# Kernel tuning notes

Measured on AMD Instinct MI355X. Metric: run time of the kernel, lower is better.

The kernel has to match this reference:

```python
import jax, jax.numpy as jnp
import numpy as np

T, H, I, E, TOP_K = 4096, 2048, 768, 16, 2


def _pack_i2s(tern):
    # tern: int8 in {-1,0,1}, shape [..., K] with K % 4 == 0
    m = (tern + 1).astype(jnp.uint8)  # map to {0,1,2}
    m = m.reshape(*tern.shape[:-1], -1, 4)
    return (m[..., 0] | (m[..., 1] << 2) | (m[..., 2] << 4) | (m[..., 3] << 6)).astype(jnp.uint8)


def _quantize_alpha(alpha):
    # per-column alpha -> int8 with global scale (quantize_alpha_int8)
    scale = jnp.maximum(jnp.abs(alpha).max(), 1e-8) / 127.0
    q = jnp.clip(jnp.round(alpha / scale), -128, 127).astype(jnp.int8)
    return q, scale.astype(jnp.float32)


def _unpack_i2s(packed, K, alpha):
    # packed: uint8 [..., N, K//4]; alpha: [..., K] per input column
    shifts = jnp.array([0, 2, 4, 6], dtype=jnp.uint8)
    ext = (packed[..., None] >> shifts) & jnp.uint8(3)  # [..., N, K//4, 4]
    vals = ext.reshape(*packed.shape[:-1], K).astype(jnp.float32) - 1.0  # {-1,0,1}
    return vals * alpha[..., None, :]


def setup_inputs() -> dict:
    key = jax.random.key(0)
    ks = jax.random.split(key, 6)
    x = jax.random.normal(ks[0], (T, H), dtype=jnp.float32)
    router_logits = jax.random.normal(ks[1], (T, E), dtype=jnp.float32)
    tern13 = jax.random.randint(ks[2], (E, 2 * I, H), -1, 2, dtype=jnp.int8)
    tern2 = jax.random.randint(ks[3], (E, H, I), -1, 2, dtype=jnp.int8)
    a13 = jax.random.uniform(ks[4], (E, H), minval=0.01, maxval=0.05, dtype=jnp.float32)
    a2 = jax.random.uniform(ks[5], (E, I), minval=0.01, maxval=0.05, dtype=jnp.float32)
    w13_alpha_q, w13_alpha_scale = _quantize_alpha(a13)
    w2_alpha_q, w2_alpha_scale = _quantize_alpha(a2)
    return {
        "x": x,
        "router_logits": router_logits,
        "w13_packed": _pack_i2s(tern13),
        "w13_alpha_q": w13_alpha_q,
        "w13_alpha_scale": w13_alpha_scale,
        "w2_packed": _pack_i2s(tern2),
        "w2_alpha_q": w2_alpha_q,
        "w2_alpha_scale": w2_alpha_scale,
    }


def reference(x, router_logits, w13_packed, w13_alpha_q, w13_alpha_scale,
              w2_packed, w2_alpha_q, w2_alpha_scale):
    # dequant int8 alphas, then dequant 2-bit ternary weights
    a13 = w13_alpha_q.astype(jnp.float32) * w13_alpha_scale  # [E, H]
    a2 = w2_alpha_q.astype(jnp.float32) * w2_alpha_scale     # [E, I]
    w13 = _unpack_i2s(w13_packed, H, a13)  # [E, 2I, H]
    w2 = _unpack_i2s(w2_packed, I, a2)     # [E, H, I]

    # top-k routing with renormalized softmax weights
    probs = jax.nn.softmax(router_logits, axis=-1)
    topw, topi = jax.lax.top_k(probs, TOP_K)           # [T, k]
    topw = topw / topw.sum(axis=-1, keepdims=True)
    combine = jnp.sum(jax.nn.one_hot(topi, E, dtype=x.dtype) * topw[..., None], axis=1)  # [T, E]

    # grouped expert matmuls (dense dispatch over experts)
    gu = jnp.einsum('th,enh->ten', x, w13)             # [T, E, 2I]
    gate, up = jnp.split(gu, 2, axis=-1)
    act = jax.nn.silu(gate) * up                       # [T, E, I]
    down = jnp.einsum('tei,ehi->teh', act, w2)         # [T, E, H]
    return jnp.einsum('te,teh->th', combine, down)     # [T, H]
```

## Files before the change

kernel.cpp:

```cpp
#include <hip/hip_runtime.h>
#include <stdint.h>

#define T_TOK 4096
#define HDIM  2048
#define IDIM  768
#define NEXP  16
#define NPAIR (T_TOK * 2)
#define PAIR_CAP (NPAIR + 256)

typedef float f32x4 __attribute__((ext_vector_type(4)));
typedef __bf16 bf16x8 __attribute__((ext_vector_type(8)));
typedef unsigned short u16x8 __attribute__((ext_vector_type(8)));
typedef unsigned int u32;
typedef const __attribute__((address_space(1))) u32* as1_u32p;
typedef __attribute__((address_space(3))) u32* as3_u32p;

__device__ __forceinline__ unsigned short f2bf(float f) {
  u32 u = __float_as_uint(f);
  u += 0x7FFFu + ((u >> 16) & 1u);
  return (unsigned short)(u >> 16);
}

__device__ __forceinline__ f32x4 mfma16(bf16x8 a, bf16x8 b, f32x4 c) {
  return __builtin_amdgcn_mfma_f32_16x16x32_bf16(a, b, c, 0, 0, 0);
}

__device__ __forceinline__ void stage16(unsigned short* dst, u32 w) {
  u32 o[8];
#pragma unroll
  for (int i = 0; i < 4; ++i) {
    const u32 t  = (w >> (2 * i)) & 0x03030303u;
    const u32 hb = __builtin_amdgcn_perm(0u, 0x003F00BFu, t);
    const u32 lb = __builtin_amdgcn_perm(0u, 0x00800080u, t);
    o[2 * i]     = __builtin_amdgcn_perm(hb, lb, 0x05010400u);
    o[2 * i + 1] = __builtin_amdgcn_perm(hb, lb, 0x07030602u);
  }
  *(uint4*)(dst + 0) = make_uint4(o[0], o[1], o[2], o[3]);
  *(uint4*)(dst + 8) = make_uint4(o[4], o[5], o[6], o[7]);
}

__global__ __launch_bounds__(256) void route_kernel(
    const float* __restrict__ logits, int* __restrict__ counts,
    int* __restrict__ t2i, float* __restrict__ t2w) {
  const int t = blockIdx.x * 256 + threadIdx.x;
  if (t >= T_TOK) return;
  const float* l = logits + t * NEXP;
  float m0 = -1e30f, m1 = -1e30f;
  int i0 = 0, i1 = 0;
#pragma unroll
  for (int j = 0; j < NEXP; ++j) {
    const float v = l[j];
    if (v > m0) { m1 = m0; i1 = i0; m0 = v; i0 = j; }
    else if (v > m1) { m1 = v; i1 = j; }
  }
  const float w0 = 1.0f / (1.0f + expf(m1 - m0));
  t2i[t] = i0 | (i1 << 8);
  t2w[t] = w0;
  atomicAdd(&counts[i0], 1);
  atomicAdd(&counts[i1], 1);
}

__global__ void scan_kernel(const int* __restrict__ counts,
                            int* __restrict__ offs, int* __restrict__ cursor) {
  if (threadIdx.x == 0) {
    int s = 0;
    for (int e = 0; e < NEXP; ++e) { offs[e] = s; cursor[e] = s; s += counts[e]; }
    offs[NEXP] = s;
  }
}

__global__ __launch_bounds__(256) void fill_kernel(
    const int* __restrict__ t2i, const float* __restrict__ t2w,
    int* __restrict__ cursor, int* __restrict__ pair_token,
    float* __restrict__ pair_wt, int* __restrict__ pair_eid,
    int* __restrict__ t2p0, int* __restrict__ t2p1) {
  const int t = blockIdx.x * 256 + threadIdx.x;
  if (t >= T_TOK) return;
  const int ii = t2i[t];
  const float w0 = t2w[t];
  const int i0 = ii & 255, i1 = (ii >> 8) & 255;
  const int p0 = atomicAdd(&cursor[i0], 1);
  pair_token[p0] = t; pair_wt[p0] = w0; pair_eid[p0] = i0;
  const int p1 = atomicAdd(&cursor[i1], 1);
  pair_token[p1] = t; pair_wt[p1] = 1.0f - w0; pair_eid[p1] = i1;
  t2p0[t] = p0; t2p1[t] = p1;
}

__global__ __launch_bounds__(256) void repack_kernel(
    const int* __restrict__ w, u32* __restrict__ o) {
  const int j0 = (blockIdx.x * 256 + threadIdx.x) * 4;
  const int4* w4 = (const int4*)w;
  uint4 r;
#pragma unroll
  for (int k = 0; k < 4; ++k) {
    const int4 a = w4[j0 + k];
    u32 x = (u32)(a.x & 255) | ((u32)(a.y & 255) << 8) |
            ((u32)(a.z & 255) << 16) | ((u32)(a.w & 255) << 24);
    u32 t = (x ^ (x >> 12)) & 0x0000F0F0u; x ^= t ^ (t << 12);
    t = (x ^ (x >> 6)) & 0x00CC00CCu;      x ^= t ^ (t << 6);
    ((u32*)&r)[k] = x;
  }
  ((uint4*)o)[blockIdx.x * 256 + threadIdx.x] = r;
}

__global__ __launch_bounds__(256) void xg_kernel(
    const float* __restrict__ x, const int* __restrict__ a13q,
    const float* __restrict__ s13p, const int* __restrict__ pair_token,
    const int* __restrict__ pair_eid, unsigned short* __restrict__ xg) {
  const int p = blockIdx.x;
  const int t = pair_token[p];
  const int e = pair_eid[p];
  const float s13 = *s13p;
  const int h0 = threadIdx.x * 8;
  const float* xp = x + (size_t)t * HDIM + h0;
  const int* ap = a13q + (size_t)e * HDIM + h0;
  const float4 x0 = ((const float4*)xp)[0];
  const float4 x1 = ((const float4*)xp)[1];
  const int4 a0 = ((const int4*)ap)[0];
  const int4 a1 = ((const int4*)ap)[1];
  u16x8 q;
  q[0] = f2bf(x0.x * (float)a0.x * s13);
  q[1] = f2bf(x0.y * (float)a0.y * s13);
  q[2] = f2bf(x0.z * (float)a0.z * s13);
  q[3] = f2bf(x0.w * (float)a0.w * s13);
  q[4] = f2bf(x1.x * (float)a1.x * s13);
  q[5] = f2bf(x1.y * (float)a1.y * s13);
  q[6] = f2bf(x1.z * (float)a1.z * s13);
  q[7] = f2bf(x1.w * (float)a1.w * s13);
  *(u16x8*)(xg + (size_t)p * HDIM + h0) = q;
}

__global__ __launch_bounds__(256, 4) void gemm1_kernel(
    const u32* __restrict__ wq13, const int* __restrict__ a2q,
    const float* __restrict__ s2p, const int* __restrict__ counts,
    const int* __restrict__ offs, const float* __restrict__ pair_wt,
    const unsigned short* __restrict__ xg, unsigned short* __restrict__ act) {
  const int id = blockIdx.x;
  const int xcd = id & 7, sblk = id >> 3;
  const int nT = sblk % 12;
  const int gg = (sblk / 12) * 8 + xcd;
  const int e = gg & 15, mT = gg >> 4;
  const int cnt = counts[e];
  if (mT * 128 >= cnt) return;
  const int base = offs[e];
  const int tid = threadIdx.x;

  __shared__ __align__(16) unsigned short sA0[128 * 32];
  __shared__ __align__(16) unsigned short sA1[128 * 32];
  __shared__ __align__(16) unsigned short sB0[128 * 40];
  __shared__ __align__(16) unsigned short sB1[128 * 40];

  const int wave = tid >> 6, lane = tid & 63;
  const int wm = wave >> 1, wn = wave & 1;
  const int quad = lane >> 4, ln = lane & 15;

  const int bn = tid >> 1, bhalf = tid & 1;
  const int grow = (bn < 64) ? (nT * 64 + bn) : (IDIM + nT * 64 + (bn - 64));
  const u32* browp = wq13 + ((size_t)e * (2 * IDIM) + grow) * (HDIM / 16);
  const int sBoff = bn * 40 + (bhalf << 4);

  const int arow = lane >> 2;
  const int acol = (lane & 3) * 8;
  const size_t arow0 = (size_t)(base + mT * 128);

  f32x4 acc[4][4] = {};

#define G1_MFMA(sAx, sBx)                                                          \
  {                                                                                \
    bf16x8 af[4];                                                                  \
    _Pragma("unroll") for (int mi = 0; mi < 4; ++mi)                               \
        af[mi] = *(const bf16x8*)(sAx + (wm * 64 + mi * 16 + ln) * 32 + quad * 8); \
    bf16x8 b0 = *(const bf16x8*)(sBx + (wn * 32 + ln) * 40 + quad * 8);            \
    bf16x8 b1 = *(const bf16x8*)(sBx + (wn * 32 + 16 + ln) * 40 + quad * 8);       \
    bf16x8 b2 = *(const bf16x8*)(sBx + (64 + wn * 32 + ln) * 40 + quad * 8);       \
    bf16x8 b3 = *(const bf16x8*)(sBx + (64 + wn * 32 + 16 + ln) * 40 + quad * 8);  \
    _Pragma("unroll") for (int mi = 0; mi < 4; ++mi) {                             \
      acc[mi][0] = mfma16(af[mi], b0, acc[mi][0]);                                 \
      acc[mi][1] = mfma16(af[mi], b1, acc[mi][1]);                                 \
      acc[mi][2] = mfma16(af[mi], b2, acc[mi][2]);                                 \
      acc[mi][3] = mfma16(af[mi], b3, acc[mi][3]);                                 \
    }                                                                              \
  }

  uint4 W = *(const uint4*)(browp);
  for (int s = 0; s < HDIM / 64; ++s) {
#pragma unroll
    for (int c = 0; c < 2; ++c) {
      const unsigned short* gp =
          xg + (arow0 + wave * 32 + c * 16 + arow) * HDIM + s * 64 + acol;
      unsigned short* lp = sA0 + (wave * 32 + c * 16) * 32;
      __builtin_amdgcn_global_load_lds((as1_u32p)(const void*)gp, (as3_u32p)(void*)lp, 16, 0, 0);
    }
#pragma unroll
    for (int c = 0; c < 2; ++c) {
      const unsigned short* gp =
          xg + (arow0 + wave * 32 + c * 16 + arow) * HDIM + s * 64 + 32 + acol;
      unsigned short* lp = sA1 + (wave * 32 + c * 16) * 32;
      __builtin_amdgcn_global_load_lds((as1_u32p)(const void*)gp, (as3_u32p)(void*)lp, 16, 0, 0);
    }
    const int sn = (s + 1 < HDIM / 64) ? s + 1 : s;
    const uint4 Wn = *(const uint4*)(browp + 4 * sn);
    stage16(sB0 + sBoff, bhalf ? W.y : W.x);
    stage16(sB1 + sBoff, bhalf ? W.w : W.z);
    __syncthreads();
    G1_MFMA(sA0, sB0);
    G1_MFMA(sA1, sB1);
    __syncthreads();
    W = Wn;
  }

  const float s2 = *s2p;
#pragma unroll
  for (int gi = 0; gi < 2; ++gi) {
    const int i = nT * 64 + wn * 32 + gi * 16 + ln;
    const float a2v = (float)a2q[e * IDIM + i] * s2;
#pragma unroll
    for (int mi = 0; mi < 4; ++mi) {
      const f32x4 g = acc[mi][gi];
      const f32x4 u = acc[mi][gi + 2];
#pragma unroll
      for (int r = 0; r < 4; ++r) {
        const int m = mT * 128 + wm * 64 + mi * 16 + quad * 4 + r;
        if (m < cnt) {
          const float wt = pair_wt[base + m];
          const float gv = g[r];
          const float av = gv / (1.0f + __expf(-gv)) * u[r] * a2v * wt;
          act[(size_t)(base + m) * IDIM + i] = f2bf(av);
        }
      }
    }
  }
}

__global__ __launch_bounds__(256, 4) void gemm2_kernel(
    const u32* __restrict__ wq2, const int* __restrict__ counts,
    const int* __restrict__ offs, const unsigned short* __restrict__ act,
    unsigned short* __restrict__ down) {
  const int id = blockIdx.x;
  const int xcd = id & 7, sblk = id >> 3;
  const int nT = sblk & 15;
  const int gg = (sblk >> 4) * 8 + xcd;
  const int e = gg & 15, mT = gg >> 4;
  const int cnt = counts[e];
  if (mT * 128 >= cnt) return;
  const int base = offs[e];
  const int tid = threadIdx.x;

  __shared__ __align__(16) unsigned short sA0[128 * 32];
  __shared__ __align__(16) unsigned short sA1[128 * 32];
  __shared__ __align__(16) unsigned short sB0[128 * 40];
  __shared__ __align__(16) unsigned short sB1[128 * 40];

  const int wave = tid >> 6, lane = tid & 63;
  const int wm = wave >> 1, wn = wave & 1;
  const int quad = lane >> 4, ln = lane & 15;

  const int bn = tid >> 1, bhalf = tid & 1;
  const u32* browp = wq2 + ((size_t)e * HDIM + nT * 128 + bn) * (IDIM / 16);
  const int sBoff = bn * 40 + (bhalf << 4);

  const int arow = lane >> 2;
  const int acol = (lane & 3) * 8;
  const size_t arow0 = (size_t)(base + mT * 128);

  f32x4 acc[4][4] = {};

#define G2_MFMA(sAx, sBx)                                                          \
  {                                                                                \
    bf16x8 af[4];                                                                  \
    _Pragma("unroll") for (int mi = 0; mi < 4; ++mi)                               \
        af[mi] = *(const bf16x8*)(sAx + (wm * 64 + mi * 16 + ln) * 32 + quad * 8); \
    bf16x8 b0 = *(const bf16x8*)(sBx + (wn * 64 + ln) * 40 + quad * 8);            \
    bf16x8 b1 = *(const bf16x8*)(sBx + (wn * 64 + 16 + ln) * 40 + quad * 8);       \
    bf16x8 b2 = *(const bf16x8*)(sBx + (wn * 64 + 32 + ln) * 40 + quad * 8);       \
    bf16x8 b3 = *(const bf16x8*)(sBx + (wn * 64 + 48 + ln) * 40 + quad * 8);       \
    _Pragma("unroll") for (int mi = 0; mi < 4; ++mi) {                             \
      acc[mi][0] = mfma16(af[mi], b0, acc[mi][0]);                                 \
      acc[mi][1] = mfma16(af[mi], b1, acc[mi][1]);                                 \
      acc[mi][2] = mfma16(af[mi], b2, acc[mi][2]);                                 \
      acc[mi][3] = mfma16(af[mi], b3, acc[mi][3]);                                 \
    }                                                                              \
  }

  uint4 W = *(const uint4*)(browp);
  for (int s = 0; s < IDIM / 64; ++s) {
#pragma unroll
    for (int c = 0; c < 2; ++c) {
      const unsigned short* gp =
          act + (arow0 + wave * 32 + c * 16 + arow) * IDIM + s * 64 + acol;
      unsigned short* lp = sA0 + (wave * 32 + c * 16) * 32;
      __builtin_amdgcn_global_load_lds((as1_u32p)(const void*)gp, (as3_u32p)(void*)lp, 16, 0, 0);
    }
#pragma unroll
    for (int c = 0; c < 2; ++c) {
      const unsigned short* gp =
          act + (arow0 + wave * 32 + c * 16 + arow) * IDIM + s * 64 + 32 + acol;
      unsigned short* lp = sA1 + (wave * 32 + c * 16) * 32;
      __builtin_amdgcn_global_load_lds((as1_u32p)(const void*)gp, (as3_u32p)(void*)lp, 16, 0, 0);
    }
    const int sn = (s + 1 < IDIM / 64) ? s + 1 : s;
    const uint4 Wn = *(const uint4*)(browp + 4 * sn);
    stage16(sB0 + sBoff, bhalf ? W.y : W.x);
    stage16(sB1 + sBoff, bhalf ? W.w : W.z);
    __syncthreads();
    G2_MFMA(sA0, sB0);
    G2_MFMA(sA1, sB1);
    __syncthreads();
    W = Wn;
  }

#pragma unroll
  for (int mi = 0; mi < 4; ++mi) {
#pragma unroll
    for (int r = 0; r < 4; ++r) {
      const int ml = wm * 64 + mi * 16 + quad * 4 + r;
      const int m = mT * 128 + ml;
      if (m < cnt) {
        unsigned short* drow = down + (size_t)(base + m) * HDIM + nT * 128 + wn * 64;
#pragma unroll
        for (int ni = 0; ni < 4; ++ni)
          drow[ni * 16 + ln] = f2bf(acc[mi][ni][r]);
      }
    }
  }
}

__global__ __launch_bounds__(256) void combine_kernel(
    const int* __restrict__ t2p0, const int* __restrict__ t2p1,
    const unsigned short* __restrict__ down, float* __restrict__ out) {
  const int t = blockIdx.x;
  const int h = threadIdx.x * 8;
  const u16x8 a = *(const u16x8*)(down + (size_t)t2p0[t] * HDIM + h);
  const u16x8 b = *(const u16x8*)(down + (size_t)t2p1[t] * HDIM + h);
  f32x4 o0, o1;
#pragma unroll
  for (int j = 0; j < 4; ++j) {
    o0[j] = __uint_as_float((u32)a[j] << 16) + __uint_as_float((u32)b[j] << 16);
    o1[j] = __uint_as_float((u32)a[j + 4] << 16) + __uint_as_float((u32)b[j + 4] << 16);
  }
  float* o = out + (size_t)t * HDIM + h;
  *(f32x4*)(o) = o0;
  *(f32x4*)(o + 4) = o1;
}

extern "C" void kernel_launch(void* const* d_in, const int* in_sizes, int n_in,
                              void* d_out, int out_size, void* d_ws, size_t ws_size,
                              hipStream_t stream) {
  const float* x      = (const float*)d_in[0];
  const float* logits = (const float*)d_in[1];
  const int*   w13p   = (const int*)d_in[2];
  const int*   a13q   = (const int*)d_in[3];
  const float* s13    = (const float*)d_in[4];
  const int*   w2p    = (const int*)d_in[5];
  const int*   a2q    = (const int*)d_in[6];
  const float* s2     = (const float*)d_in[7];
  float* out = (float*)d_out;

  char* ws = (char*)d_ws;
  int*   counts     = (int*)(ws + 0);
  int*   cursor     = (int*)(ws + 64);
  int*   offs       = (int*)(ws + 128);
  int*   t2i        = (int*)(ws + 256);
  float* t2w        = (float*)(ws + 256 + 4 * T_TOK);
  int*   t2p0       = (int*)(ws + 256 + 8 * T_TOK);
  int*   t2p1       = (int*)(ws + 256 + 12 * T_TOK);
  int*   pair_token = (int*)(ws + 256 + 16 * T_TOK);
  float* pair_wt    = (float*)(ws + 256 + 16 * T_TOK + 4 * PAIR_CAP);
  int*   pair_eid   = (int*)(ws + 256 + 16 * T_TOK + 8 * PAIR_CAP);
  const size_t hdr_end = ((size_t)(256 + 16 * T_TOK + 12 * PAIR_CAP) + 255) & ~(size_t)255;

  const size_t n32_13 = (size_t)NEXP * 2 * IDIM * (HDIM / 16);
  const size_t n32_2  = (size_t)NEXP * HDIM * (IDIM / 16);
  const size_t rp13_b = n32_13 * 4, rp2_b = n32_2 * 4;
  const size_t xg_b   = (size_t)PAIR_CAP * HDIM * 2;

  u32* rp13 = (u32*)(ws + hdr_end);
  u32* rp2  = (u32*)(ws + hdr_end + rp13_b);
  unsigned short* xg  = (unsigned short*)(ws + hdr_end + rp13_b + rp2_b);
  unsigned short* act = (unsigned short*)(ws + hdr_end + rp13_b + rp2_b + xg_b);
  unsigned short* down = xg;

  hipMemsetAsync(counts, 0, 256, stream);
  route_kernel<<<T_TOK / 256, 256, 0, stream>>>(logits, counts, t2i, t2w);
  scan_kernel<<<1, 64, 0, stream>>>(counts, offs, cursor);
  fill_kernel<<<T_TOK / 256, 256, 0, stream>>>(t2i, t2w, cursor, pair_token, pair_wt,
                                               pair_eid, t2p0, t2p1);
  repack_kernel<<<(int)(n32_13 / 1024), 256, 0, stream>>>(w13p, rp13);
  repack_kernel<<<(int)(n32_2 / 1024), 256, 0, stream>>>(w2p, rp2);
  xg_kernel<<<NPAIR, 256, 0, stream>>>(x, a13q, s13, pair_token, pair_eid, xg);

  gemm1_kernel<<<6144, 256, 0, stream>>>(rp13, a2q, s2, counts, offs, pair_wt, xg, act);
  gemm2_kernel<<<8192, 256, 0, stream>>>(rp2, counts, offs, act, down);
  combine_kernel<<<T_TOK, 256, 0, stream>>>(t2p0, t2p1, down, out);
}
```

Baseline: 335.6 us.

## Expand ternary B fragments in registers and double-buffer A tiles in LDS

Both expert GEMM kernels stop staging decoded ternary weights through shared memory. Each lane now loads the packed words it needs and expands them straight into MFMA B fragments, which removes the LDS write/read round trip for B and one barrier per step. The LDS saved is spent on double-buffering the activation tiles: the async global-to-LDS copy for the next K step is issued before the current step's MFMAs, and s_setprio raises the priority of the MFMA block. In exchange, each wave reloads and re-expands weight rows that other waves also use, and register pressure rises, so the launch bound drops from 4 to 3 blocks per CU.

```diff
diff --git a/kernel.cpp b/kernel.cpp
--- a/kernel.cpp
+++ b/kernel.cpp
@@ -12,6 +12,7 @@
 typedef __bf16 bf16x8 __attribute__((ext_vector_type(8)));
 typedef unsigned short u16x8 __attribute__((ext_vector_type(8)));
 typedef unsigned int u32;
+typedef u32 u32x4 __attribute__((ext_vector_type(4)));
 typedef const __attribute__((address_space(1))) u32* as1_u32p;
 typedef __attribute__((address_space(3))) u32* as3_u32p;
 
@@ -25,18 +26,20 @@
   return __builtin_amdgcn_mfma_f32_16x16x32_bf16(a, b, c, 0, 0, 0);
 }
 
-__device__ __forceinline__ void stage16(unsigned short* dst, u32 w) {
-  u32 o[8];
-#pragma unroll
-  for (int i = 0; i < 4; ++i) {
-    const u32 t  = (w >> (2 * i)) & 0x03030303u;
-    const u32 hb = __builtin_amdgcn_perm(0u, 0x003F00BFu, t);
-    const u32 lb = __builtin_amdgcn_perm(0u, 0x00800080u, t);
-    o[2 * i]     = __builtin_amdgcn_perm(hb, lb, 0x05010400u);
-    o[2 * i + 1] = __builtin_amdgcn_perm(hb, lb, 0x07030602u);
-  }
-  *(uint4*)(dst + 0) = make_uint4(o[0], o[1], o[2], o[3]);
-  *(uint4*)(dst + 8) = make_uint4(o[4], o[5], o[6], o[7]);
+__device__ __forceinline__ bf16x8 expand8(u32 w, int qshift) {
+  w >>= qshift;
+  const u32 t0 = w & 0x03030303u;
+  const u32 h0 = __builtin_amdgcn_perm(0u, 0x003F00BFu, t0);
+  const u32 l0 = __builtin_amdgcn_perm(0u, 0x00800080u, t0);
+  const u32 t1 = (w >> 2) & 0x03030303u;
+  const u32 h1 = __builtin_amdgcn_perm(0u, 0x003F00BFu, t1);
+  const u32 l1 = __builtin_amdgcn_perm(0u, 0x00800080u, t1);
+  u32x4 o;
+  o[0] = __builtin_amdgcn_perm(h0, l0, 0x05010400u);
+  o[1] = __builtin_amdgcn_perm(h0, l0, 0x07030602u);
+  o[2] = __builtin_amdgcn_perm(h1, l1, 0x05010400u);
+  o[3] = __builtin_amdgcn_perm(h1, l1, 0x07030602u);
+  return __builtin_bit_cast(bf16x8, o);
 }
 
 __global__ __launch_bounds__(256) void route_kernel(
@@ -130,7 +133,59 @@
   *(u16x8*)(xg + (size_t)p * HDIM + h0) = q;
 }
 
-__global__ __launch_bounds__(256, 4) void gemm1_kernel(
+#define DMA_A(src, pitch, dst0, dst1, sidx)                                          \
+  {                                                                                  \
+    _Pragma("unroll") for (int c = 0; c < 2; ++c) {                                  \
+      const unsigned short* gp =                                                     \
+          src + (arow0 + wave * 32 + c * 16 + arow) * (pitch) + (sidx) * 64 + acol;  \
+      unsigned short* lp = dst0 + (wave * 32 + c * 16) * 32;                         \
+      __builtin_amdgcn_global_load_lds((as1_u32p)(const void*)gp,                    \
+                                       (as3_u32p)(void*)lp, 16, 0, 0);               \
+    }                                                                                \
+    _Pragma("unroll") for (int c = 0; c < 2; ++c) {                                  \
+      const unsigned short* gp =                                                     \
+          src + (arow0 + wave * 32 + c * 16 + arow) * (pitch) + (sidx) * 64 + 32 +   \
+          acol;                                                                      \
+      unsigned short* lp = dst1 + (wave * 32 + c * 16) * 32;                         \
+      __builtin_amdgcn_global_load_lds((as1_u32p)(const void*)gp,                    \
+                                       (as3_u32p)(void*)lp, 16, 0, 0);               \
+    }                                                                                \
+  }
+
+#define LOADW(W0, W1, W2, W3, sidx)            \
+  {                                            \
+    W0 = *(const uint4*)(rp0 + (sidx) * 4);    \
+    W1 = *(const uint4*)(rp1 + (sidx) * 4);    \
+    W2 = *(const uint4*)(rp2 + (sidx) * 4);    \
+    W3 = *(const uint4*)(rp3 + (sidx) * 4);    \
+  }
+
+#define MKFRAGS(fr, W0, W1, W2, W3)                       \
+  {                                                       \
+    fr[0] = expand8(qsel ? W0.y : W0.x, qshift);          \
+    fr[1] = expand8(qsel ? W1.y : W1.x, qshift);          \
+    fr[2] = expand8(qsel ? W2.y : W2.x, qshift);          \
+    fr[3] = expand8(qsel ? W3.y : W3.x, qshift);          \
+    fr[4] = expand8(qsel ? W0.w : W0.z, qshift);          \
+    fr[5] = expand8(qsel ? W1.w : W1.z, qshift);          \
+    fr[6] = expand8(qsel ? W2.w : W2.z, qshift);          \
+    fr[7] = expand8(qsel ? W3.w : W3.z, qshift);          \
+  }
+
+#define MFMA4(sAx, b0, b1, b2, b3)                                                  \
+  {                                                                                 \
+    bf16x8 af[4];                                                                   \
+    _Pragma("unroll") for (int mi = 0; mi < 4; ++mi)                                \
+        af[mi] = *(const bf16x8*)(sAx + (wm * 64 + mi * 16 + ln) * 32 + quad * 8);  \
+    _Pragma("unroll") for (int mi = 0; mi < 4; ++mi) {                              \
+      acc[mi][0] = mfma16(af[mi], b0, acc[mi][0]);                                  \
+      acc[mi][1] = mfma16(af[mi], b1, acc[mi][1]);                                  \
+      acc[mi][2] = mfma16(af[mi], b2, acc[mi][2]);                                  \
+      acc[mi][3] = mfma16(af[mi], b3, acc[mi][3]);                                  \
+    }                                                                               \
+  }
+
+__global__ __launch_bounds__(256, 3) void gemm1_kernel(
     const u32* __restrict__ wq13, const int* __restrict__ a2q,
     const float* __restrict__ s2p, const int* __restrict__ counts,
     const int* __restrict__ offs, const float* __restrict__ pair_wt,
@@ -145,19 +200,19 @@
   const int base = offs[e];
   const int tid = threadIdx.x;
 
-  __shared__ __align__(16) unsigned short sA0[128 * 32];
-  __shared__ __align__(16) unsigned short sA1[128 * 32];
-  __shared__ __align__(16) unsigned short sB0[128 * 40];
-  __shared__ __align__(16) unsigned short sB1[128 * 40];
+  __shared__ __align__(16) unsigned short sA[2][2][128 * 32];
 
   const int wave = tid >> 6, lane = tid & 63;
   const int wm = wave >> 1, wn = wave & 1;
   const int quad = lane >> 4, ln = lane & 15;
-
-  const int bn = tid >> 1, bhalf = tid & 1;
-  const int grow = (bn < 64) ? (nT * 64 + bn) : (IDIM + nT * 64 + (bn - 64));
-  const u32* browp = wq13 + ((size_t)e * (2 * IDIM) + grow) * (HDIM / 16);
-  const int sBoff = bn * 40 + (bhalf << 4);
+  const int qsel = quad >> 1;
+  const int qshift = (quad & 1) * 4;
+
+  const size_t rstride = HDIM / 16;
+  const u32* rp0 = wq13 + ((size_t)e * (2 * IDIM) + nT * 64 + wn * 32 + ln) * rstride;
+  const u32* rp1 = rp0 + 16 * rstride;
+  const u32* rp2 = rp0 + (size_t)IDIM * rstride;
+  const u32* rp3 = rp2 + 16 * rstride;
 
   const int arow = lane >> 2;
   const int acol = (lane & 3) * 8;
@@ -165,55 +220,45 @@
 
   f32x4 acc[4][4] = {};
 
-#define G1_MFMA(sAx, sBx)                                                          \
-  {                                                                                \
-    bf16x8 af[4];                                                                  \
-    _Pragma("unroll") for (int mi = 0; mi < 4; ++mi)                               \
-        af[mi] = *(const bf16x8*)(sAx + (wm * 64 + mi * 16 + ln) * 32 + quad * 8); \
-    bf16x8 b0 = *(const bf16x8*)(sBx + (wn * 32 + ln) * 40 + quad * 8);            \
-    bf16x8 b1 = *(const bf16x8*)(sBx + (wn * 32 + 16 + ln) * 40 + quad * 8);       \
-    bf16x8 b2 = *(const bf16x8*)(sBx + (64 + wn * 32 + ln) * 40 + quad * 8);       \
-    bf16x8 b3 = *(const bf16x8*)(sBx + (64 + wn * 32 + 16 + ln) * 40 + quad * 8);  \
-    _Pragma("unroll") for (int mi = 0; mi < 4; ++mi) {                             \
-      acc[mi][0] = mfma16(af[mi], b0, acc[mi][0]);                                 \
-      acc[mi][1] = mfma16(af[mi], b1, acc[mi][1]);                                 \
-      acc[mi][2] = mfma16(af[mi], b2, acc[mi][2]);                                 \
-      acc[mi][3] = mfma16(af[mi], b3, acc[mi][3]);                                 \
-    }                                                                              \
-  }
-
-  uint4 W = *(const uint4*)(browp);
-  for (int s = 0; s < HDIM / 64; ++s) {
-#pragma unroll
-    for (int c = 0; c < 2; ++c) {
-      const unsigned short* gp =
-          xg + (arow0 + wave * 32 + c * 16 + arow) * HDIM + s * 64 + acol;
-      unsigned short* lp = sA0 + (wave * 32 + c * 16) * 32;
-      __builtin_amdgcn_global_load_lds((as1_u32p)(const void*)gp, (as3_u32p)(void*)lp, 16, 0, 0);
-    }
-#pragma unroll
-    for (int c = 0; c < 2; ++c) {
-      const unsigned short* gp =
-          xg + (arow0 + wave * 32 + c * 16 + arow) * HDIM + s * 64 + 32 + acol;
-      unsigned short* lp = sA1 + (wave * 32 + c * 16) * 32;
-      __builtin_amdgcn_global_load_lds((as1_u32p)(const void*)gp, (as3_u32p)(void*)lp, 16, 0, 0);
-    }
-    const int sn = (s + 1 < HDIM / 64) ? s + 1 : s;
-    const uint4 Wn = *(const uint4*)(browp + 4 * sn);
-    stage16(sB0 + sBoff, bhalf ? W.y : W.x);
-    stage16(sB1 + sBoff, bhalf ? W.w : W.z);
-    __syncthreads();
-    G1_MFMA(sA0, sB0);
-    G1_MFMA(sA1, sB1);
-    __syncthreads();
-    W = Wn;
-  }
-
-  const float s2 = *s2p;
+  DMA_A(xg, HDIM, sA[0][0], sA[0][1], 0);
+  uint4 WA0, WA1, WA2, WA3, WB0, WB1, WB2, WB3;
+  LOADW(WA0, WA1, WA2, WA3, 0);
+  LOADW(WB0, WB1, WB2, WB3, 1);
+
+  const int S2 = (HDIM / 64) / 2;
+  for (int s2 = 0; s2 < S2; ++s2) {
+    const int s = 2 * s2;
+    {
+      bf16x8 fr[8];
+      MKFRAGS(fr, WA0, WA1, WA2, WA3);
+      __syncthreads();
+      DMA_A(xg, HDIM, sA[1][0], sA[1][1], s + 1);
+      if (s2 + 1 < S2) LOADW(WA0, WA1, WA2, WA3, s + 2);
+      __builtin_amdgcn_s_setprio(1);
+      MFMA4(sA[0][0], fr[0], fr[1], fr[2], fr[3]);
+      MFMA4(sA[0][1], fr[4], fr[5], fr[6], fr[7]);
+      __builtin_amdgcn_s_setprio(0);
+    }
+    {
+      bf16x8 fr[8];
+      MKFRAGS(fr, WB0, WB1, WB2, WB3);
+      __syncthreads();
+      if (s2 + 1 < S2) {
+        DMA_A(xg, HDIM, sA[0][0], sA[0][1], s + 2);
+        LOADW(WB0, WB1, WB2, WB3, s + 3);
+      }
+      __builtin_amdgcn_s_setprio(1);
+      MFMA4(sA[1][0], fr[0], fr[1], fr[2], fr[3]);
+      MFMA4(sA[1][1], fr[4], fr[5], fr[6], fr[7]);
+      __builtin_amdgcn_s_setprio(0);
+    }
+  }
+
+  const float s2v = *s2p;
 #pragma unroll
   for (int gi = 0; gi < 2; ++gi) {
     const int i = nT * 64 + wn * 32 + gi * 16 + ln;
-    const float a2v = (float)a2q[e * IDIM + i] * s2;
+    const float a2v = (float)a2q[e * IDIM + i] * s2v;
 #pragma unroll
     for (int mi = 0; mi < 4; ++mi) {
       const f32x4 g = acc[mi][gi];
@@ -232,7 +277,7 @@
   }
 }
 
-__global__ __launch_bounds__(256, 4) void gemm2_kernel(
+__global__ __launch_bounds__(256, 3) void gemm2_kernel(
     const u32* __restrict__ wq2, const int* __restrict__ counts,
     const int* __restrict__ offs, const unsigned short* __restrict__ act,
     unsigned short* __restrict__ down) {
@@ -246,18 +291,19 @@
   const int base = offs[e];
   const int tid = threadIdx.x;
 
-  __shared__ __align__(16) unsigned short sA0[128 * 32];
-  __shared__ __align__(16) unsigned short sA1[128 * 32];
-  __shared__ __align__(16) unsigned short sB0[128 * 40];
-  __shared__ __align__(16) unsigned short sB1[128 * 40];
+  __shared__ __align__(16) unsigned short sA[2][2][128 * 32];
 
   const int wave = tid >> 6, lane = tid & 63;
   const int wm = wave >> 1, wn = wave & 1;
   const int quad = lane >> 4, ln = lane & 15;
-
-  const int bn = tid >> 1, bhalf = tid & 1;
-  const u32* browp = wq2 + ((size_t)e * HDIM + nT * 128 + bn) * (IDIM / 16);
-  const int sBoff = bn * 40 + (bhalf << 4);
+  const int qsel = quad >> 1;
+  const int qshift = (quad & 1) * 4;
+
+  const size_t rstride = IDIM / 16;
+  const u32* rp0 = wq2 + ((size_t)e * HDIM + nT * 128 + wn * 64 + ln) * rstride;
+  const u32* rp1 = rp0 + 16 * rstride;
+  const u32* rp2 = rp0 + 32 * rstride;
+  const u32* rp3 = rp0 + 48 * rstride;
 
   const int arow = lane >> 2;
   const int acol = (lane & 3) * 8;
@@ -265,48 +311,38 @@
 
   f32x4 acc[4][4] = {};
 
-#define G2_MFMA(sAx, sBx)                                                          \
-  {                                                                                \
-    bf16x8 af[4];                                                                  \
-    _Pragma("unroll") for (int mi = 0; mi < 4; ++mi)                               \
-        af[mi] = *(const bf16x8*)(sAx + (wm * 64 + mi * 16 + ln) * 32 + quad * 8); \
-    bf16x8 b0 = *(const bf16x8*)(sBx + (wn * 64 + ln) * 40 + quad * 8);            \
-    bf16x8 b1 = *(const bf16x8*)(sBx + (wn * 64 + 16 + ln) * 40 + quad * 8);       \
-    bf16x8 b2 = *(const bf16x8*)(sBx + (wn * 64 + 32 + ln) * 40 + quad * 8);       \
-    bf16x8 b3 = *(const bf16x8*)(sBx + (wn * 64 + 48 + ln) * 40 + quad * 8);       \
-    _Pragma("unroll") for (int mi = 0; mi < 4; ++mi) {                             \
-      acc[mi][0] = mfma16(af[mi], b0, acc[mi][0]);                                 \
-      acc[mi][1] = mfma16(af[mi], b1, acc[mi][1]);                                 \
-      acc[mi][2] = mfma16(af[mi], b2, acc[mi][2]);                                 \
-      acc[mi][3] = mfma16(af[mi], b3, acc[mi][3]);                                 \
-    }                                                                              \
-  }
-
-  uint4 W = *(const uint4*)(browp);
-  for (int s = 0; s < IDIM / 64; ++s) {
-#pragma unroll
-    for (int c = 0; c < 2; ++c) {
-      const unsigned short* gp =
-          act + (arow0 + wave * 32 + c * 16 + arow) * IDIM + s * 64 + acol;
-      unsigned short* lp = sA0 + (wave * 32 + c * 16) * 32;
-      __builtin_amdgcn_global_load_lds((as1_u32p)(const void*)gp, (as3_u32p)(void*)lp, 16, 0, 0);
-    }
-#pragma unroll
-    for (int c = 0; c < 2; ++c) {
-      const unsigned short* gp =
-          act + (arow0 + wave * 32 + c * 16 + arow) * IDIM + s * 64 + 32 + acol;
-      unsigned short* lp = sA1 + (wave * 32 + c * 16) * 32;
-      __builtin_amdgcn_global_load_lds((as1_u32p)(const void*)gp, (as3_u32p)(void*)lp, 16, 0, 0);
-    }
-    const int sn = (s + 1 < IDIM / 64) ? s + 1 : s;
-    const uint4 Wn = *(const uint4*)(browp + 4 * sn);
-    stage16(sB0 + sBoff, bhalf ? W.y : W.x);
-    stage16(sB1 + sBoff, bhalf ? W.w : W.z);
-    __syncthreads();
-    G2_MFMA(sA0, sB0);
-    G2_MFMA(sA1, sB1);
-    __syncthreads();
-    W = Wn;
+  DMA_A(act, IDIM, sA[0][0], sA[0][1], 0);
+  uint4 WA0, WA1, WA2, WA3, WB0, WB1, WB2, WB3;
+  LOADW(WA0, WA1, WA2, WA3, 0);
+  LOADW(WB0, WB1, WB2, WB3, 1);
+
+  const int S2 = (IDIM / 64) / 2;
+  for (int s2 = 0; s2 < S2; ++s2) {
+    const int s = 2 * s2;
+    {
+      bf16x8 fr[8];
+      MKFRAGS(fr, WA0, WA1, WA2, WA3);
+      __syncthreads();
+      DMA_A(act, IDIM, sA[1][0], sA[1][1], s + 1);
+      if (s2 + 1 < S2) LOADW(WA0, WA1, WA2, WA3, s + 2);
+      __builtin_amdgcn_s_setprio(1);
+      MFMA4(sA[0][0], fr[0], fr[1], fr[2], fr[3]);
+      MFMA4(sA[0][1], fr[4], fr[5], fr[6], fr[7]);
+      __builtin_amdgcn_s_setprio(0);
+    }
+    {
+      bf16x8 fr[8];
+      MKFRAGS(fr, WB0, WB1, WB2, WB3);
+      __syncthreads();
+      if (s2 + 1 < S2) {
+        DMA_A(act, IDIM, sA[0][0], sA[0][1], s + 2);
+        LOADW(WB0, WB1, WB2, WB3, s + 3);
+      }
+      __builtin_amdgcn_s_setprio(1);
+      MFMA4(sA[1][0], fr[0], fr[1], fr[2], fr[3]);
+      MFMA4(sA[1][1], fr[4], fr[5], fr[6], fr[7]);
+      __builtin_amdgcn_s_setprio(0);
+    }
   }
 
 #pragma unroll
```

Measured after the change: 386.7 us. +15.2%, slower.

## Double-buffer A tiles with async LDS DMA and raise MFMA priority in both GEMMs

Applied to the files above, without the earlier changes.

Both expert GEMM kernels now double-buffer the activation A tiles in LDS. The next k-step's global_load_lds DMA is issued right after the barrier, so it overlaps with the current step's MFMAs instead of being waited on in the same iteration. The MFMA sections are wrapped in s_setprio to favour the matrix work, and occupancy hints change from launch_bounds(256,4) to waves_per_eu(3,3). The extra A buffer adds 16KB of LDS per block, which may reduce resident blocks per CU.

```diff
diff --git a/kernel.cpp b/kernel.cpp
--- a/kernel.cpp
+++ b/kernel.cpp
@@ -12,6 +12,7 @@
 typedef __bf16 bf16x8 __attribute__((ext_vector_type(8)));
 typedef unsigned short u16x8 __attribute__((ext_vector_type(8)));
 typedef unsigned int u32;
+typedef u32 u32x4 __attribute__((ext_vector_type(4)));
 typedef const __attribute__((address_space(1))) u32* as1_u32p;
 typedef __attribute__((address_space(3))) u32* as3_u32p;
 
@@ -130,40 +131,28 @@
   *(u16x8*)(xg + (size_t)p * HDIM + h0) = q;
 }
 
-__global__ __launch_bounds__(256, 4) void gemm1_kernel(
-    const u32* __restrict__ wq13, const int* __restrict__ a2q,
-    const float* __restrict__ s2p, const int* __restrict__ counts,
-    const int* __restrict__ offs, const float* __restrict__ pair_wt,
-    const unsigned short* __restrict__ xg, unsigned short* __restrict__ act) {
-  const int id = blockIdx.x;
-  const int xcd = id & 7, sblk = id >> 3;
-  const int nT = sblk % 12;
-  const int gg = (sblk / 12) * 8 + xcd;
-  const int e = gg & 15, mT = gg >> 4;
-  const int cnt = counts[e];
-  if (mT * 128 >= cnt) return;
-  const int base = offs[e];
-  const int tid = threadIdx.x;
-
-  __shared__ __align__(16) unsigned short sA0[128 * 32];
-  __shared__ __align__(16) unsigned short sA1[128 * 32];
-  __shared__ __align__(16) unsigned short sB0[128 * 40];
-  __shared__ __align__(16) unsigned short sB1[128 * 40];
-
-  const int wave = tid >> 6, lane = tid & 63;
-  const int wm = wave >> 1, wn = wave & 1;
-  const int quad = lane >> 4, ln = lane & 15;
-
-  const int bn = tid >> 1, bhalf = tid & 1;
-  const int grow = (bn < 64) ? (nT * 64 + bn) : (IDIM + nT * 64 + (bn - 64));
-  const u32* browp = wq13 + ((size_t)e * (2 * IDIM) + grow) * (HDIM / 16);
-  const int sBoff = bn * 40 + (bhalf << 4);
-
-  const int arow = lane >> 2;
-  const int acol = (lane & 3) * 8;
-  const size_t arow0 = (size_t)(base + mT * 128);
-
-  f32x4 acc[4][4] = {};
+#define DMA_A(src, pitch, dst0, dst1, sidx)                                          \
+  {                                                                                  \
+    _Pragma("unroll") for (int c = 0; c < 2; ++c) {                                  \
+      const unsigned short* gp =                                                     \
+          src + (arow0 + wave * 32 + c * 16 + arow) * (pitch) + (sidx) * 64 + acol;  \
+      unsigned short* lp = dst0 + (wave * 32 + c * 16) * 32;                         \
+      __builtin_amdgcn_global_load_lds((as1_u32p)(const void*)gp,                    \
+                                       (as3_u32p)(void*)lp, 16, 0, 0);               \
+    }                                                                                \
+    _Pragma("unroll") for (int c = 0; c < 2; ++c) {                                  \
+      const unsigned short* gp =                                                     \
+          src + (arow0 + wave * 32 + c * 16 + arow) * (pitch) + (sidx) * 64 + 32 +   \
+          acol;                                                                      \
+      unsigned short* lp = dst1 + (wave * 32 + c * 16) * 32;                         \
+      __builtin_amdgcn_global_load_lds((as1_u32p)(const void*)gp,                    \
+                                       (as3_u32p)(void*)lp, 16, 0, 0);               \
+    }                                                                                \
+  }
+
+#define STAGE(W)                                   \
+  stage16(sB0 + sBoff, bhalf ? (W).y : (W).x);     \
+  stage16(sB1 + sBoff, bhalf ? (W).w : (W).z);
 
 #define G1_MFMA(sAx, sBx)                                                          \
   {                                                                                \
@@ -182,38 +171,79 @@
     }                                                                              \
   }
 
-  uint4 W = *(const uint4*)(browp);
-  for (int s = 0; s < HDIM / 64; ++s) {
-#pragma unroll
-    for (int c = 0; c < 2; ++c) {
-      const unsigned short* gp =
-          xg + (arow0 + wave * 32 + c * 16 + arow) * HDIM + s * 64 + acol;
-      unsigned short* lp = sA0 + (wave * 32 + c * 16) * 32;
-      __builtin_amdgcn_global_load_lds((as1_u32p)(const void*)gp, (as3_u32p)(void*)lp, 16, 0, 0);
-    }
-#pragma unroll
-    for (int c = 0; c < 2; ++c) {
-      const unsigned short* gp =
-          xg + (arow0 + wave * 32 + c * 16 + arow) * HDIM + s * 64 + 32 + acol;
-      unsigned short* lp = sA1 + (wave * 32 + c * 16) * 32;
-      __builtin_amdgcn_global_load_lds((as1_u32p)(const void*)gp, (as3_u32p)(void*)lp, 16, 0, 0);
-    }
-    const int sn = (s + 1 < HDIM / 64) ? s + 1 : s;
-    const uint4 Wn = *(const uint4*)(browp + 4 * sn);
-    stage16(sB0 + sBoff, bhalf ? W.y : W.x);
-    stage16(sB1 + sBoff, bhalf ? W.w : W.z);
-    __syncthreads();
-    G1_MFMA(sA0, sB0);
-    G1_MFMA(sA1, sB1);
-    __syncthreads();
-    W = Wn;
-  }
-
-  const float s2 = *s2p;
+__attribute__((amdgpu_waves_per_eu(3, 3))) __global__ __launch_bounds__(256)
+void gemm1_kernel(
+    const u32* __restrict__ wq13, const int* __restrict__ a2q,
+    const float* __restrict__ s2p, const int* __restrict__ counts,
+    const int* __restrict__ offs, const float* __restrict__ pair_wt,
+    const unsigned short* __restrict__ xg, unsigned short* __restrict__ act) {
+  const int id = blockIdx.x;
+  const int xcd = id & 7, sblk = id >> 3;
+  const int nT = sblk % 12;
+  const int gg = (sblk / 12) * 8 + xcd;
+  const int e = gg & 15, mT = gg >> 4;
+  const int cnt = counts[e];
+  if (mT * 128 >= cnt) return;
+  const int base = offs[e];
+  const int tid = threadIdx.x;
+
+  __shared__ __align__(16) unsigned short sA[2][2][128 * 32];
+  __shared__ __align__(16) unsigned short sB0[128 * 40 + 8];
+  __shared__ __align__(16) unsigned short sB1[128 * 40 + 8];
+
+  const int wave = tid >> 6, lane = tid & 63;
+  const int wm = wave >> 1, wn = wave & 1;
+  const int quad = lane >> 4, ln = lane & 15;
+
+  const int bn = tid >> 1, bhalf = tid & 1;
+  const int grow = (bn < 64) ? (nT * 64 + bn) : (IDIM + nT * 64 + (bn - 64));
+  const u32* browp = wq13 + ((size_t)e * (2 * IDIM) + grow) * (HDIM / 16);
+  const int sBoff = bn * 40 + (bhalf << 4);
+
+  const int arow = lane >> 2;
+  const int acol = (lane & 3) * 8;
+  const size_t arow0 = (size_t)(base + mT * 128);
+
+  f32x4 acc[4][4] = {};
+
+  DMA_A(xg, HDIM, sA[0][0], sA[0][1], 0);
+  uint4 WA = *(const uint4*)(browp);
+  uint4 WB;
+
+  const int S2 = (HDIM / 64) / 2;
+  for (int s2i = 0; s2i < S2; ++s2i) {
+    const int s = 2 * s2i;
+    {
+      STAGE(WA);
+      __syncthreads();
+      DMA_A(xg, HDIM, sA[1][0], sA[1][1], s + 1);
+      WB = *(const uint4*)(browp + 4 * (s + 1));
+      __builtin_amdgcn_s_setprio(1);
+      G1_MFMA(sA[0][0], sB0);
+      G1_MFMA(sA[0][1], sB1);
+      __builtin_amdgcn_s_setprio(0);
+      __syncthreads();
+    }
+    {
+      STAGE(WB);
+      __syncthreads();
+      if (s2i + 1 < S2) {
+        DMA_A(xg, HDIM, sA[0][0], sA[0][1], s + 2);
+        WA = *(const uint4*)(browp + 4 * (s + 2));
+      }
+      __builtin_amdgcn_s_setprio(1);
+      G1_MFMA(sA[1][0], sB0);
+      G1_MFMA(sA[1][1], sB1);
+      __builtin_amdgcn_s_setprio(0);
+      __syncthreads();
+    }
+  }
+
+  const float s2v = *s2p;
 #pragma unroll
   for (int gi = 0; gi < 2; ++gi) {
     const int i = nT * 64 + wn * 32 + gi * 16 + ln;
-    const float a2v = (float)a2q[e * IDIM + i] * s2;
+    const float a2v = (float)a2q[e * IDIM + i] * s2v;
 #pragma unroll
     for (int mi = 0; mi < 4; ++mi) {
       const f32x4 g = acc[mi][gi];
@@ -231,39 +261,6 @@
     }
   }
 }
-
-__global__ __launch_bounds__(256, 4) void gemm2_kernel(
-    const u32* __restrict__ wq2, const int* __restrict__ counts,
-    const int* __restrict__ offs, const unsigned short* __restrict__ act,
-    unsigned short* __restrict__ down) {
-  const int id = blockIdx.x;
-  const int xcd = id & 7, sblk = id >> 3;
-  const int nT = sblk & 15;
-  const int gg = (sblk >> 4) * 8 + xcd;
-  const int e = gg & 15, mT = gg >> 4;
-  const int cnt = counts[e];
-  if (mT * 128 >= cnt) return;
-  const int base = offs[e];
-  const int tid = threadIdx.x;
-
-  __shared__ __align__(16) unsigned short sA0[128 * 32];
-  __shared__ __align__(16) unsigned short sA1[128 * 32];
-  __shared__ __align__(16) unsigned short sB0[128 * 40];
-  __shared__ __align__(16) unsigned short sB1[128 * 40];
-
-  const int wave = tid >> 6, lane = tid & 63;
-  const int wm = wave >> 1, wn = wave & 1;
-  const int quad = lane >> 4, ln = lane & 15;
-
-  const int bn = tid >> 1, bhalf = tid & 1;
-  const u32* browp = wq2 + ((size_t)e * HDIM + nT * 128 + bn) * (IDIM / 16);
-  const int sBoff = bn * 40 + (bhalf << 4);
-
-  const int arow = lane >> 2;
-  const int acol = (lane & 3) * 8;
-  const size_t arow0 = (size_t)(base + mT * 128);
-
-  f32x4 acc[4][4] = {};
 
 #define G2_MFMA(sAx, sBx)                                                          \
   {                                                                                \
@@ -282,31 +279,70 @@
     }                                                                              \
   }
 
-  uint4 W = *(const uint4*)(browp);
-  for (int s = 0; s < IDIM / 64; ++s) {
-#pragma unroll
-    for (int c = 0; c < 2; ++c) {
-      const unsigned short* gp =
-          act + (arow0 + wave * 32 + c * 16 + arow) * IDIM + s * 64 + acol;
-      unsigned short* lp = sA0 + (wave * 32 + c * 16) * 32;
-      __builtin_amdgcn_global_load_lds((as1_u32p)(const void*)gp, (as3_u32p)(void*)lp, 16, 0, 0);
-    }
-#pragma unroll
-    for (int c = 0; c < 2; ++c) {
-      const unsigned short* gp =
-          act + (arow0 + wave * 32 + c * 16 + arow) * IDIM + s * 64 + 32 + acol;
-      unsigned short* lp = sA1 + (wave * 32 + c * 16) * 32;
-      __builtin_amdgcn_global_load_lds((as1_u32p)(const void*)gp, (as3_u32p)(void*)lp, 16, 0, 0);
-    }
-    const int sn = (s + 1 < IDIM / 64) ? s + 1 : s;
-    const uint4 Wn = *(const uint4*)(browp + 4 * sn);
-    stage16(sB0 + sBoff, bhalf ? W.y : W.x);
-    stage16(sB1 + sBoff, bhalf ? W.w : W.z);
-    __syncthreads();
-    G2_MFMA(sA0, sB0);
-    G2_MFMA(sA1, sB1);
-    __syncthreads();
-    W = Wn;
+__attribute__((amdgpu_waves_per_eu(3, 3))) __global__ __launch_bounds__(256)
+void gemm2_kernel(
+    const u32* __restrict__ wq2, const int* __restrict__ counts,
+    const int* __restrict__ offs, const unsigned short* __restrict__ act,
+    unsigned short* __restrict__ down) {
+  const int id = blockIdx.x;
+  const int xcd = id & 7, sblk = id >> 3;
+  const int nT = sblk & 15;
+  const int gg = (sblk >> 4) * 8 + xcd;
+  const int e = gg & 15, mT = gg >> 4;
+  const int cnt = counts[e];
+  if (mT * 128 >= cnt) return;
+  const int base = offs[e];
+  const int tid = threadIdx.x;
+
+  __shared__ __align__(16) unsigned short sA[2][2][128 * 32];
+  __shared__ __align__(16) unsigned short sB0[128 * 40 + 8];
+  __shared__ __align__(16) unsigned short sB1[128 * 40 + 8];
+
+  const int wave = tid >> 6, lane = tid & 63;
+  const int wm = wave >> 1, wn = wave & 1;
+  const int quad = lane >> 4, ln = lane & 15;
+
+  const int bn = tid >> 1, bhalf = tid & 1;
+  const u32* browp = wq2 + ((size_t)e * HDIM + nT * 128 + bn) * (IDIM / 16);
+  const int sBoff = bn * 40 + (bhalf << 4);
+
+  const int arow = lane >> 2;
+  const int acol = (lane & 3) * 8;
+  const size_t arow0 = (size_t)(base + mT * 128);
+
+  f32x4 acc[4][4] = {};
+
+  DMA_A(act, IDIM, sA[0][0], sA[0][1], 0);
+  uint4 WA = *(const uint4*)(browp);
+  uint4 WB;
+
+  const int S2 = (IDIM / 64) / 2;
+  for (int s2i = 0; s2i < S2; ++s2i) {
+    const int s = 2 * s2i;
+    {
+      STAGE(WA);
+      __syncthreads();
+      DMA_A(act, IDIM, sA[1][0], sA[1][1], s + 1);
+      WB = *(const uint4*)(browp + 4 * (s + 1));
+      __builtin_amdgcn_s_setprio(1);
+      G2_MFMA(sA[0][0], sB0);
+      G2_MFMA(sA[0][1], sB1);
+      __builtin_amdgcn_s_setprio(0);
+      __syncthreads();
+    }
+    {
+      STAGE(WB);
+      __syncthreads();
+      if (s2i + 1 < S2) {
+        DMA_A(act, IDIM, sA[0][0], sA[0][1], s + 2);
+        WA = *(const uint4*)(browp + 4 * (s + 2));
+      }
+      __builtin_amdgcn_s_setprio(1);
+      G2_MFMA(sA[1][0], sB0);
+      G2_MFMA(sA[1][1], sB1);
+      __builtin_amdgcn_s_setprio(0);
+      __syncthreads();
+    }
   }
 
 #pragma unroll
```

New measurement: 362.3 us. +8.0%, slower.

## Software-pipeline both expert GEMMs with ping-pong K-half LDS buffers and MFMA priority

Applied to the files above, without the earlier changes.

Restructures the K loop of both grouped GEMM kernels so that the DMA of A and the ternary staging of B into one LDS buffer overlap with MFMA on the other buffer, in 32-wide K halves. The previous version loaded a full 64-wide step and then waited on a barrier before computing. It also raises wave priority around the MFMA blocks with s_setprio. The rework adds a barrier between halves, and its correctness depends on global_load_lds completing before the next barrier.

```diff
diff --git a/kernel.cpp b/kernel.cpp
--- a/kernel.cpp
+++ b/kernel.cpp
@@ -130,6 +130,51 @@
   *(u16x8*)(xg + (size_t)p * HDIM + h0) = q;
 }
 
+#define DMA_A32(src, pitch, dst, sidx)                                               \
+  {                                                                                  \
+    _Pragma("unroll") for (int c = 0; c < 2; ++c) {                                  \
+      const unsigned short* gp =                                                     \
+          src + (arow0 + wave * 32 + c * 16 + arow) * (pitch) + (sidx) * 32 + acol;  \
+      unsigned short* lp = dst + (wave * 32 + c * 16) * 32;                          \
+      __builtin_amdgcn_global_load_lds((as1_u32p)(const void*)gp,                    \
+                                       (as3_u32p)(void*)lp, 16, 0, 0);               \
+    }                                                                                \
+  }
+
+#define G1_MFMA32(sAx, sBx)                                                        \
+  {                                                                                \
+    bf16x8 af[4];                                                                  \
+    _Pragma("unroll") for (int mi = 0; mi < 4; ++mi)                               \
+        af[mi] = *(const bf16x8*)(sAx + (wm * 64 + mi * 16 + ln) * 32 + quad * 8); \
+    bf16x8 b0 = *(const bf16x8*)(sBx + (wn * 32 + ln) * 40 + quad * 8);            \
+    bf16x8 b1 = *(const bf16x8*)(sBx + (wn * 32 + 16 + ln) * 40 + quad * 8);       \
+    bf16x8 b2 = *(const bf16x8*)(sBx + (64 + wn * 32 + ln) * 40 + quad * 8);       \
+    bf16x8 b3 = *(const bf16x8*)(sBx + (64 + wn * 32 + 16 + ln) * 40 + quad * 8);  \
+    _Pragma("unroll") for (int mi = 0; mi < 4; ++mi) {                             \
+      acc[mi][0] = mfma16(af[mi], b0, acc[mi][0]);                                 \
+      acc[mi][1] = mfma16(af[mi], b1, acc[mi][1]);                                 \
+      acc[mi][2] = mfma16(af[mi], b2, acc[mi][2]);                                 \
+      acc[mi][3] = mfma16(af[mi], b3, acc[mi][3]);                                 \
+    }                                                                              \
+  }
+
+#define G2_MFMA32(sAx, sBx)                                                        \
+  {                                                                                \
+    bf16x8 af[4];                                                                  \
+    _Pragma("unroll") for (int mi = 0; mi < 4; ++mi)                               \
+        af[mi] = *(const bf16x8*)(sAx + (wm * 64 + mi * 16 + ln) * 32 + quad * 8); \
+    bf16x8 b0 = *(const bf16x8*)(sBx + (wn * 64 + ln) * 40 + quad * 8);            \
+    bf16x8 b1 = *(const bf16x8*)(sBx + (wn * 64 + 16 + ln) * 40 + quad * 8);       \
+    bf16x8 b2 = *(const bf16x8*)(sBx + (wn * 64 + 32 + ln) * 40 + quad * 8);       \
+    bf16x8 b3 = *(const bf16x8*)(sBx + (wn * 64 + 48 + ln) * 40 + quad * 8);       \
+    _Pragma("unroll") for (int mi = 0; mi < 4; ++mi) {                             \
+      acc[mi][0] = mfma16(af[mi], b0, acc[mi][0]);                                 \
+      acc[mi][1] = mfma16(af[mi], b1, acc[mi][1]);                                 \
+      acc[mi][2] = mfma16(af[mi], b2, acc[mi][2]);                                 \
+      acc[mi][3] = mfma16(af[mi], b3, acc[mi][3]);                                 \
+    }                                                                              \
+  }
+
 __global__ __launch_bounds__(256, 4) void gemm1_kernel(
     const u32* __restrict__ wq13, const int* __restrict__ a2q,
     const float* __restrict__ s2p, const int* __restrict__ counts,
@@ -145,10 +190,8 @@
   const int base = offs[e];
   const int tid = threadIdx.x;
 
-  __shared__ __align__(16) unsigned short sA0[128 * 32];
-  __shared__ __align__(16) unsigned short sA1[128 * 32];
-  __shared__ __align__(16) unsigned short sB0[128 * 40];
-  __shared__ __align__(16) unsigned short sB1[128 * 40];
+  __shared__ __align__(16) unsigned short sA[2][128 * 32];
+  __shared__ __align__(16) unsigned short sB[2][128 * 40 + 8];
 
   const int wave = tid >> 6, lane = tid & 63;
   const int wm = wave >> 1, wn = wave & 1;
@@ -156,7 +199,7 @@
 
   const int bn = tid >> 1, bhalf = tid & 1;
   const int grow = (bn < 64) ? (nT * 64 + bn) : (IDIM + nT * 64 + (bn - 64));
-  const u32* browp = wq13 + ((size_t)e * (2 * IDIM) + grow) * (HDIM / 16);
+  const uint4* browp4 = (const uint4*)(wq13 + ((size_t)e * (2 * IDIM) + grow) * (HDIM / 16));
   const int sBoff = bn * 40 + (bhalf << 4);
 
   const int arow = lane >> 2;
@@ -165,55 +208,36 @@
 
   f32x4 acc[4][4] = {};
 
-#define G1_MFMA(sAx, sBx)                                                          \
-  {                                                                                \
-    bf16x8 af[4];                                                                  \
-    _Pragma("unroll") for (int mi = 0; mi < 4; ++mi)                               \
-        af[mi] = *(const bf16x8*)(sAx + (wm * 64 + mi * 16 + ln) * 32 + quad * 8); \
-    bf16x8 b0 = *(const bf16x8*)(sBx + (wn * 32 + ln) * 40 + quad * 8);            \
-    bf16x8 b1 = *(const bf16x8*)(sBx + (wn * 32 + 16 + ln) * 40 + quad * 8);       \
-    bf16x8 b2 = *(const bf16x8*)(sBx + (64 + wn * 32 + ln) * 40 + quad * 8);       \
-    bf16x8 b3 = *(const bf16x8*)(sBx + (64 + wn * 32 + 16 + ln) * 40 + quad * 8);  \
-    _Pragma("unroll") for (int mi = 0; mi < 4; ++mi) {                             \
-      acc[mi][0] = mfma16(af[mi], b0, acc[mi][0]);                                 \
-      acc[mi][1] = mfma16(af[mi], b1, acc[mi][1]);                                 \
-      acc[mi][2] = mfma16(af[mi], b2, acc[mi][2]);                                 \
-      acc[mi][3] = mfma16(af[mi], b3, acc[mi][3]);                                 \
-    }                                                                              \
-  }
-
-  uint4 W = *(const uint4*)(browp);
-  for (int s = 0; s < HDIM / 64; ++s) {
-#pragma unroll
-    for (int c = 0; c < 2; ++c) {
-      const unsigned short* gp =
-          xg + (arow0 + wave * 32 + c * 16 + arow) * HDIM + s * 64 + acol;
-      unsigned short* lp = sA0 + (wave * 32 + c * 16) * 32;
-      __builtin_amdgcn_global_load_lds((as1_u32p)(const void*)gp, (as3_u32p)(void*)lp, 16, 0, 0);
+  DMA_A32(xg, HDIM, sA[0], 0);
+  uint4 WA = browp4[0];
+  stage16(sB[0] + sBoff, bhalf ? WA.y : WA.x);
+  uint4 WN;
+
+  const int S2 = (HDIM / 32) / 2;
+  for (int j = 0; j < S2; ++j) {
+    __syncthreads();
+    DMA_A32(xg, HDIM, sA[1], 2 * j + 1);
+    if (j + 1 < S2) WN = browp4[j + 1];
+    stage16(sB[1] + sBoff, bhalf ? WA.w : WA.z);
+    __builtin_amdgcn_s_setprio(1);
+    G1_MFMA32(sA[0], sB[0]);
+    __builtin_amdgcn_s_setprio(0);
+    __syncthreads();
+    if (j + 1 < S2) {
+      DMA_A32(xg, HDIM, sA[0], 2 * j + 2);
+      stage16(sB[0] + sBoff, bhalf ? WN.y : WN.x);
     }
-#pragma unroll
-    for (int c = 0; c < 2; ++c) {
-      const unsigned short* gp =
-          xg + (arow0 + wave * 32 + c * 16 + arow) * HDIM + s * 64 + 32 + acol;
-      unsigned short* lp = sA1 + (wave * 32 + c * 16) * 32;
-      __builtin_amdgcn_global_load_lds((as1_u32p)(const void*)gp, (as3_u32p)(void*)lp, 16, 0, 0);
-    }
-    const int sn = (s + 1 < HDIM / 64) ? s + 1 : s;
-    const uint4 Wn = *(const uint4*)(browp + 4 * sn);
-    stage16(sB0 + sBoff, bhalf ? W.y : W.x);
-    stage16(sB1 + sBoff, bhalf ? W.w : W.z);
-    __syncthreads();
-    G1_MFMA(sA0, sB0);
-    G1_MFMA(sA1, sB1);
-    __syncthreads();
-    W = Wn;
-  }
-
-  const float s2 = *s2p;
+    __builtin_amdgcn_s_setprio(1);
+    G1_MFMA32(sA[1], sB[1]);
+    __builtin_amdgcn_s_setprio(0);
+    WA = WN;
+  }
+
+  const float s2v = *s2p;
 #pragma unroll
   for (int gi = 0; gi < 2; ++gi) {
     const int i = nT * 64 + wn * 32 + gi * 16 + ln;
-    const float a2v = (float)a2q[e * IDIM + i] * s2;
+    const float a2v = (float)a2q[e * IDIM + i] * s2v;
 #pragma unroll
     for (int mi = 0; mi < 4; ++mi) {
       const f32x4 g = acc[mi][gi];
@@ -246,17 +270,15 @@
   const int base = offs[e];
   const int tid = threadIdx.x;
 
-  __shared__ __align__(16) unsigned short sA0[128 * 32];
-  __shared__ __align__(16) unsigned short sA1[128 * 32];
-  __shared__ __align__(16) unsigned short sB0[128 * 40];
-  __shared__ __align__(16) unsigned short sB1[128 * 40];
+  __shared__ __align__(16) unsigned short sA[2][128 * 32];
+  __shared__ __align__(16) unsigned short sB[2][128 * 40 + 8];
 
   const int wave = tid >> 6, lane = tid & 63;
   const int wm = wave >> 1, wn = wave & 1;
   const int quad = lane >> 4, ln = lane & 15;
 
   const int bn = tid >> 1, bhalf = tid & 1;
-  const u32* browp = wq2 + ((size_t)e * HDIM + nT * 128 + bn) * (IDIM / 16);
+  const uint4* browp4 = (const uint4*)(wq2 + ((size_t)e * HDIM + nT * 128 + bn) * (IDIM / 16));
   const int sBoff = bn * 40 + (bhalf << 4);
 
   const int arow = lane >> 2;
@@ -265,48 +287,29 @@
 
   f32x4 acc[4][4] = {};
 
-#define G2_MFMA(sAx, sBx)                                                          \
-  {                                                                                \
-    bf16x8 af[4];                                                                  \
-    _Pragma("unroll") for (int mi = 0; mi < 4; ++mi)                               \
-        af[mi] = *(const bf16x8*)(sAx + (wm * 64 + mi * 16 + ln) * 32 + quad * 8); \
-    bf16x8 b0 = *(const bf16x8*)(sBx + (wn * 64 + ln) * 40 + quad * 8);            \
-    bf16x8 b1 = *(const bf16x8*)(sBx + (wn * 64 + 16 + ln) * 40 + quad * 8);       \
-    bf16x8 b2 = *(const bf16x8*)(sBx + (wn * 64 + 32 + ln) * 40 + quad * 8);       \
-    bf16x8 b3 = *(const bf16x8*)(sBx + (wn * 64 + 48 + ln) * 40 + quad * 8);       \
-    _Pragma("unroll") for (int mi = 0; mi < 4; ++mi) {                             \
-      acc[mi][0] = mfma16(af[mi], b0, acc[mi][0]);                                 \
-      acc[mi][1] = mfma16(af[mi], b1, acc[mi][1]);                                 \
-      acc[mi][2] = mfma16(af[mi], b2, acc[mi][2]);                                 \
-      acc[mi][3] = mfma16(af[mi], b3, acc[mi][3]);                                 \
-    }                                                                              \
-  }
-
-  uint4 W = *(const uint4*)(browp);
-  for (int s = 0; s < IDIM / 64; ++s) {
-#pragma unroll
-    for (int c = 0; c < 2; ++c) {
-      const unsigned short* gp =
-          act + (arow0 + wave * 32 + c * 16 + arow) * IDIM + s * 64 + acol;
-      unsigned short* lp = sA0 + (wave * 32 + c * 16) * 32;
-      __builtin_amdgcn_global_load_lds((as1_u32p)(const void*)gp, (as3_u32p)(void*)lp, 16, 0, 0);
+  DMA_A32(act, IDIM, sA[0], 0);
+  uint4 WA = browp4[0];
+  stage16(sB[0] + sBoff, bhalf ? WA.y : WA.x);
+  uint4 WN;
+
+  const int S2 = (IDIM / 32) / 2;
+  for (int j = 0; j < S2; ++j) {
+    __syncthreads();
+    DMA_A32(act, IDIM, sA[1], 2 * j + 1);
+    if (j + 1 < S2) WN = browp4[j + 1];
+    stage16(sB[1] + sBoff, bhalf ? WA.w : WA.z);
+    __builtin_amdgcn_s_setprio(1);
+    G2_MFMA32(sA[0], sB[0]);
+    __builtin_amdgcn_s_setprio(0);
+    __syncthreads();
+    if (j + 1 < S2) {
+      DMA_A32(act, IDIM, sA[0], 2 * j + 2);
+      stage16(sB[0] + sBoff, bhalf ? WN.y : WN.x);
     }
-#pragma unroll
-    for (int c = 0; c < 2; ++c) {
-      const unsigned short* gp =
-          act + (arow0 + wave * 32 + c * 16 + arow) * IDIM + s * 64 + 32 + acol;
-      unsigned short* lp = sA1 + (wave * 32 + c * 16) * 32;
-      __builtin_amdgcn_global_load_lds((as1_u32p)(const void*)gp, (as3_u32p)(void*)lp, 16, 0, 0);
-    }
-    const int sn = (s + 1 < IDIM / 64) ? s + 1 : s;
-    const uint4 Wn = *(const uint4*)(browp + 4 * sn);
-    stage16(sB0 + sBoff, bhalf ? W.y : W.x);
-    stage16(sB1 + sBoff, bhalf ? W.w : W.z);
-    __syncthreads();
-    G2_MFMA(sA0, sB0);
-    G2_MFMA(sA1, sB1);
-    __syncthreads();
-    W = Wn;
+    __builtin_amdgcn_s_setprio(1);
+    G2_MFMA32(sA[1], sB[1]);
+    __builtin_amdgcn_s_setprio(0);
+    WA = WN;
   }
 
 #pragma unroll
```

New measurement: 336.9 us. No clear change (+0.4%).
